# Kernel optimization log

Hardware: AMD Instinct MI355X
Metric: run time of the kernel (lower is better)

Reference implementation:

```python
import jax, jax.numpy as jnp
import numpy as np
from jax import lax

B, K, S = 1, 4, 1024
D = 1024          # hidden_size
DI = 2048         # intermediate_size = 2*D (expand=2)
N = 16            # ssm state size
DT_RANK = 64      # ceil(D/16)
CONV_K = 4
N_LAYERS = 48
CARD = 2048       # vocab
EPS = 1e-5


def setup_inputs() -> dict:
    key = jax.random.key(0)
    ks = jax.random.split(key, 10)
    sc = 0.02
    sequence = jax.random.randint(ks[0], (B, K, S), 0, CARD)
    emb_W = jax.random.normal(ks[1], (K, CARD, D), jnp.float32) * sc
    norm_w = jnp.ones((N_LAYERS, D), jnp.float32)
    in_W = jax.random.normal(ks[2], (N_LAYERS, 2 * DI, D), jnp.float32) * sc
    conv_w = jax.random.normal(ks[3], (N_LAYERS, DI, CONV_K), jnp.float32) * sc
    conv_b = jnp.zeros((N_LAYERS, DI), jnp.float32)
    x_W = jax.random.normal(ks[4], (N_LAYERS, DT_RANK + 2 * N, DI), jnp.float32) * sc
    dt_W = jax.random.normal(ks[5], (N_LAYERS, DI, DT_RANK), jnp.float32) * sc
    dt_b = jax.random.normal(ks[6], (N_LAYERS, DI), jnp.float32) * 0.1
    # HF Mamba init: A_log = log([1..N]) broadcast over channels
    A_log = jnp.log(jnp.broadcast_to(jnp.arange(1, N + 1, dtype=jnp.float32), (N_LAYERS, DI, N)))
    D_skip = jnp.ones((N_LAYERS, DI), jnp.float32)
    out_W = jax.random.normal(ks[7], (N_LAYERS, D, DI), jnp.float32) * sc
    normf_w = jnp.ones((D,), jnp.float32)
    head_W = jax.random.normal(ks[8], (K, CARD, D), jnp.float32) * sc
    head_b = jnp.zeros((K, CARD), jnp.float32)
    return {"sequence": sequence, "emb_W": emb_W, "norm_w": norm_w, "in_W": in_W,
            "conv_w": conv_w, "conv_b": conv_b, "x_W": x_W, "dt_W": dt_W, "dt_b": dt_b,
            "A_log": A_log, "D_skip": D_skip, "out_W": out_W, "normf_w": normf_w,
            "head_W": head_W, "head_b": head_b}


def rmsnorm(x, w):
    return x * lax.rsqrt(jnp.mean(x * x, -1, keepdims=True) + EPS) * w


def mamba_block(x, p):
    """One HF MambaBlock: residual + RMSNorm + MambaMixer (selective scan)."""
    norm_w, in_W, conv_w, conv_b, x_W, dt_W, dt_b, A_log, D_skip, out_W = p
    res = x
    h = rmsnorm(x, norm_w)
    proj = h @ in_W.T                                  # (B,S,2*DI)
    xz, gate = jnp.split(proj, 2, axis=-1)
    # causal depthwise conv1d, kernel 4
    xc = jnp.transpose(xz, (0, 2, 1))                  # (B,DI,S)
    xc = lax.conv_general_dilated(xc, conv_w[:, None, :], (1,), [(CONV_K - 1, 0)],
                                  feature_group_count=DI,
                                  dimension_numbers=("NCH", "OIH", "NCH"))
    xc = xc + conv_b[None, :, None]
    u = jax.nn.silu(jnp.transpose(xc, (0, 2, 1)))      # (B,S,DI)
    ssm_in = u @ x_W.T                                 # (B,S,DT_RANK+2N)
    dt_r, Bm, Cm = jnp.split(ssm_in, [DT_RANK, DT_RANK + N], axis=-1)
    dt = jax.nn.softplus(dt_r @ dt_W.T + dt_b)         # (B,S,DI)
    A = -jnp.exp(A_log)                                # (DI,N)

    def step(hst, inp):
        dt_t, B_t, C_t, u_t = inp                      # (B,DI),(B,N),(B,N),(B,DI)
        dA = jnp.exp(dt_t[:, :, None] * A)             # (B,DI,N)
        hst = dA * hst + (dt_t * u_t)[:, :, None] * B_t[:, None, :]
        y = jnp.einsum("bdn,bn->bd", hst, C_t)
        return hst, y

    h0 = jnp.zeros((B, DI, N), x.dtype)
    _, ys = lax.scan(step, h0, (dt.swapaxes(0, 1), Bm.swapaxes(0, 1),
                                Cm.swapaxes(0, 1), u.swapaxes(0, 1)))
    y = ys.swapaxes(0, 1) + u * D_skip                 # (B,S,DI)
    y = y * jax.nn.silu(gate)
    return res + y @ out_W.T


mamba_block_ckpt = jax.checkpoint(mamba_block)


def reference(sequence, emb_W, norm_w, in_W, conv_w, conv_b, x_W, dt_W, dt_b,
              A_log, D_skip, out_W, normf_w, head_W, head_b):
    # sum of K token-stream embeddings
    x = emb_W[jnp.arange(K)[None, :, None], sequence].sum(1)   # (B,S,D)

    def layer(x, p):
        return mamba_block_ckpt(x, p), None

    x, _ = lax.scan(layer, x, (norm_w, in_W, conv_w, conv_b, x_W, dt_W, dt_b,
                               A_log, D_skip, out_W))
    x = rmsnorm(x, normf_w)
    logits = jnp.einsum("bsd,kvd->bksv", x, head_W) + head_b[None, :, None, :]
    return logits                                              # (B,K,S,CARD)
```

## Files before the change

### kernel.cpp

```cpp
#include <hip/hip_runtime.h>
#include <hip/hip_bf16.h>

#define S 1024
#define D 1024
#define DI 2048
#define NSTATE 16
#define DTR 64
#define XPD 96
#define NL 48
#define CARD 2048
#define KTOK 4

typedef __attribute__((ext_vector_type(8))) short bf16x8;
typedef __attribute__((ext_vector_type(4))) float f32x4;
struct __align__(16) US8 { unsigned long long a, b; };

__device__ __forceinline__ unsigned short f2bf(float f) {
    unsigned u = __builtin_bit_cast(unsigned, f);
    return (unsigned short)((u + 0x7fffu + ((u >> 16) & 1u)) >> 16);
}
__device__ __forceinline__ float bf2f(unsigned short u) {
    return __builtin_bit_cast(float, (unsigned)u << 16);
}
__device__ __forceinline__ float fsilu(float x) { return x / (1.f + __expf(-x)); }
__device__ __forceinline__ float fsoftplus(float x) {
    return fmaxf(x, 0.f) + log1pf(__expf(-fabsf(x)));
}
template<int CTRL>
__device__ __forceinline__ float dpp_add(float v) {
    int m = __builtin_amdgcn_update_dpp(0, __builtin_bit_cast(int, v), CTRL, 0xF, 0xF, true);
    return v + __builtin_bit_cast(float, m);
}
__device__ __forceinline__ void gload_lds16(const void* g, void* l) {
    __builtin_amdgcn_global_load_lds((const __attribute__((address_space(1))) void*)g,
                                     (__attribute__((address_space(3))) void*)l, 16, 0, 0);
}
template<int N> __device__ __forceinline__ void wait_vm() {
    if constexpr (N == 0)      asm volatile("s_waitcnt vmcnt(0)" ::: "memory");
    else if constexpr (N == 3) asm volatile("s_waitcnt vmcnt(3)" ::: "memory");
    else if constexpr (N == 4) asm volatile("s_waitcnt vmcnt(4)" ::: "memory");
    else if constexpr (N == 6) asm volatile("s_waitcnt vmcnt(6)" ::: "memory");
    else                       asm volatile("s_waitcnt vmcnt(8)" ::: "memory");
}

__global__ __launch_bounds__(256) void cvt4_kernel(const float* __restrict__ a, long NA,
                                                   const float* __restrict__ b, long NB,
                                                   const float* __restrict__ c, long NC,
                                                   const float* __restrict__ d, long ND,
                                                   unsigned short* __restrict__ oa,
                                                   unsigned short* __restrict__ ob,
                                                   unsigned short* __restrict__ oc,
                                                   unsigned short* __restrict__ od) {
    long i = (long)blockIdx.x * 256 + threadIdx.x;
    const float* src; unsigned short* dst; long off;
    if (i < NA)                    { src = a; dst = oa; off = i; }
    else if (i < NA + NB)          { src = b; dst = ob; off = i - NA; }
    else if (i < NA + NB + NC)     { src = c; dst = oc; off = i - NA - NB; }
    else                            { src = d; dst = od; off = i - NA - NB - NC; }
    f32x4 v0 = *(const f32x4*)&src[off * 8];
    f32x4 v1 = *(const f32x4*)&src[off * 8 + 4];
    US8 pk;
    pk.a = (unsigned long long)f2bf(v0[0]) | ((unsigned long long)f2bf(v0[1]) << 16)
         | ((unsigned long long)f2bf(v0[2]) << 32) | ((unsigned long long)f2bf(v0[3]) << 48);
    pk.b = (unsigned long long)f2bf(v1[0]) | ((unsigned long long)f2bf(v1[1]) << 16)
         | ((unsigned long long)f2bf(v1[2]) << 32) | ((unsigned long long)f2bf(v1[3]) << 48);
    *(US8*)&dst[off * 8] = pk;
}

__global__ __launch_bounds__(256) void embed_kernel(const int* __restrict__ seq,
                                                    const float* __restrict__ embW,
                                                    float* __restrict__ x) {
    int s = blockIdx.x, t = threadIdx.x;
    f32x4 acc = (f32x4)0.f;
#pragma unroll
    for (int k = 0; k < KTOK; ++k) {
        int tok = seq[k * S + s];
        const f32x4 v = *(const f32x4*)&embW[((size_t)k * CARD + tok) * D + t * 4];
        acc += v;
    }
    *(f32x4*)&x[(size_t)s * D + t * 4] = acc;
}

__global__ __launch_bounds__(256) void rmsnorm_kernel(const float* __restrict__ x,
                                                      const float* __restrict__ w,
                                                      unsigned short* __restrict__ o) {
    int row = blockIdx.x, t = threadIdx.x;
    f32x4 v = *(const f32x4*)&x[(size_t)row * D + t * 4];
    float ss = v[0]*v[0] + v[1]*v[1] + v[2]*v[2] + v[3]*v[3];
#pragma unroll
    for (int off = 32; off >= 1; off >>= 1) ss += __shfl_xor(ss, off);
    __shared__ float red[4];
    int wave = t >> 6, lane = t & 63;
    if (lane == 0) red[wave] = ss;
    __syncthreads();
    ss = red[0] + red[1] + red[2] + red[3];
    float rs = rsqrtf(ss * (1.f / D) + 1e-5f);
    f32x4 wv = *(const f32x4*)&w[t * 4];
    unsigned long long pk = 0;
#pragma unroll
    for (int j = 0; j < 4; ++j)
        pk |= (unsigned long long)f2bf(v[j] * rs * wv[j]) << (16 * j);
    *(unsigned long long*)&o[(size_t)row * D + t * 4] = pk;
}

__global__ __launch_bounds__(256) void outred_rms_kernel(const float* __restrict__ part,
                                                         float* __restrict__ x,
                                                         const float* __restrict__ w,
                                                         unsigned short* __restrict__ o) {
    int row = blockIdx.x, t = threadIdx.x;
    size_t base = (size_t)row * D + t * 4;
    f32x4 v = *(const f32x4*)&x[base];
#pragma unroll
    for (int j = 0; j < 2; ++j)
        v += *(const f32x4*)&part[(size_t)j * (S * D) + base];
    *(f32x4*)&x[base] = v;
    float ss = v[0]*v[0] + v[1]*v[1] + v[2]*v[2] + v[3]*v[3];
#pragma unroll
    for (int off = 32; off >= 1; off >>= 1) ss += __shfl_xor(ss, off);
    __shared__ float red[4];
    int wave = t >> 6, lane = t & 63;
    if (lane == 0) red[wave] = ss;
    __syncthreads();
    ss = red[0] + red[1] + red[2] + red[3];
    float rs = rsqrtf(ss * (1.f / D) + 1e-5f);
    f32x4 wv = *(const f32x4*)&w[t * 4];
    unsigned long long pk = 0;
#pragma unroll
    for (int j = 0; j < 4; ++j)
        pk |= (unsigned long long)f2bf(v[j] * rs * wv[j]) << (16 * j);
    *(unsigned long long*)&o[base] = pk;
}

__global__ __launch_bounds__(256) void ssm_reduce_kernel(const float* __restrict__ part,
                                                         float* __restrict__ ssm,
                                                         unsigned short* __restrict__ ssmb) {
    int i = blockIdx.x * 256 + threadIdx.x;
    float a = 0.f;
#pragma unroll
    for (int j = 0; j < 8; ++j)
        a += part[(size_t)j * (S * XPD) + i];
    ssm[i] = a;
    ssmb[i] = f2bf(a);
}

__global__ __launch_bounds__(256) void conv_silu_kernel(const float* __restrict__ proj,
                                                        const float* __restrict__ cw,
                                                        const float* __restrict__ cb,
                                                        unsigned short* __restrict__ ub) {
    int idx = blockIdx.x * 256 + threadIdx.x;
    int s = idx >> 11, c = idx & (DI - 1);
    f32x4 w = *(const f32x4*)&cw[c * 4];
    float acc = cb[c];
#pragma unroll
    for (int t = 0; t < 4; ++t) {
        int ss = s - 3 + t;
        if (ss >= 0) acc = fmaf(w[t], proj[(size_t)ss * 4096 + c], acc);
    }
    ub[idx] = f2bf(acc * (1.f / (1.f + __expf(-acc))));
}

__global__ __launch_bounds__(1024, 2) void scan2_kernel(const unsigned short* __restrict__ ssmb,
                                                        const unsigned short* __restrict__ dtWb,
                                                        const float* __restrict__ dtb,
                                                        const unsigned short* __restrict__ ub,
                                                        const float* __restrict__ ssm,
                                                        const float* __restrict__ proj,
                                                        const float* __restrict__ A_log,
                                                        const float* __restrict__ Dsk,
                                                        unsigned short* __restrict__ yfb) {
    __shared__ float sdu[S * 4 * 2];
    __shared__ float sP[1024], sQ[1024];

    const int tid = threadIdx.x;
    const int d0 = blockIdx.x * 4;
    const int chunk = tid >> 6;
    const int lane = tid & 63;
    const int dl = (tid >> 4) & 3;
    const int n = tid & 15;
    const int sbase = chunk * 64;

#pragma unroll
    for (int i = 0; i < 4; ++i) {
        int idx = tid + i * 1024;
        int s = idx >> 2, d2 = idx & 3;
        sdu[idx * 2 + 1] = bf2f(ub[(size_t)s * DI + d0 + d2]);
    }

    {
        const int lr = lane & 15;
        const int lk = (lane >> 4) << 3;
        f32x4 dacc[4];
#pragma unroll
        for (int m = 0; m < 4; ++m) dacc[m] = (f32x4)0.f;
        bf16x8 wf0 = *(const bf16x8*)&dtWb[(size_t)(d0 + lr) * DTR + lk];
        bf16x8 wf1 = *(const bf16x8*)&dtWb[(size_t)(d0 + lr) * DTR + 32 + lk];
#pragma unroll
        for (int m = 0; m < 4; ++m) {
            const unsigned short* arow = &ssmb[(size_t)(sbase + m * 16 + lr) * XPD];
            bf16x8 a0 = *(const bf16x8*)&arow[lk];
            bf16x8 a1 = *(const bf16x8*)&arow[32 + lk];
            dacc[m] = __builtin_amdgcn_mfma_f32_16x16x32_bf16(a0, wf0, dacc[m], 0, 0, 0);
            dacc[m] = __builtin_amdgcn_mfma_f32_16x16x32_bf16(a1, wf1, dacc[m], 0, 0, 0);
        }
        if (lr < 4) {
            float bias = dtb[d0 + lr];
            const int rb = (lane >> 4) << 2;
#pragma unroll
            for (int m = 0; m < 4; ++m)
#pragma unroll
                for (int j = 0; j < 4; ++j) {
                    int sl = sbase + m * 16 + rb + j;
                    sdu[(sl * 4 + lr) * 2 + 0] = fsoftplus(dacc[m][j] + bias);
                }
        }
    }
    const float Av = -__expf(A_log[(d0 + dl) * NSTATE + n]);
    const float Dv = Dsk[d0 + dl];
    __syncthreads();

    float h = 0.f, P = 1.f;
#pragma unroll 4
    for (int i = 0; i < 64; ++i) {
        int s = sbase + i;
        float2 du = *(const float2*)&sdu[(s * 4 + dl) * 2];
        float Bs  = ssm[s * XPD + DTR + n];
        float dA  = __expf(du.x * Av);
        P *= dA;
        h = fmaf(dA, h, du.x * du.y * Bs);
    }
    const int pqb = (dl * 16 + n) * 16;
    sP[pqb + chunk] = P;
    sQ[pqb + chunk] = h;
    __syncthreads();
    float hi = 0.f;
    for (int j = 0; j < chunk; ++j) hi = fmaf(sP[pqb + j], hi, sQ[pqb + j]);
    h = hi;
#pragma unroll 2
    for (int i = 0; i < 64; ++i) {
        int s = sbase + i;
        float2 du = *(const float2*)&sdu[(s * 4 + dl) * 2];
        float Bs  = ssm[s * XPD + DTR + n];
        float Cs  = ssm[s * XPD + DTR + NSTATE + n];
        float dA  = __expf(du.x * Av);
        h = fmaf(dA, h, du.x * du.y * Bs);
        float pc = h * Cs;
        pc = dpp_add<0xB1>(pc);
        pc = dpp_add<0x4E>(pc);
        pc = dpp_add<0x124>(pc);
        pc = dpp_add<0x128>(pc);
        if (n == 0) {
            float g = proj[(size_t)s * 4096 + 2048 + d0 + dl];
            yfb[(size_t)s * DI + d0 + dl] = f2bf((pc + du.y * Dv) * fsilu(g));
        }
    }
}

template<int MR, int NR, int EPI, int KSPLIT, int ABF16, int DBUF>
__global__ __launch_bounds__(256) void gemm_bt(const void* __restrict__ Av, int lda,
                                               const unsigned short* __restrict__ W,
                                               float* __restrict__ C,
                                               int K, int N,
                                               const float* __restrict__ bias) {
    constexpr int BM = MR * 32;
    constexpr int BN = NR * 32;
    static_assert(DBUF == 0 || ((BM == 64 || BM == 128) && BN == 128 && ABF16 == 1), "dbuf shape");
    constexpr int NBUF = DBUF ? 3 : 1;
    __shared__ unsigned short As[NBUF][BM][32];
    __shared__ unsigned short Ws[NBUF][BN][32];
    const int tid = threadIdx.x;
    const int lane = tid & 63;
    const int wave = tid >> 6;
    const int wr = wave >> 1, wc = wave & 1;
    const int m0 = blockIdx.y * BM;
    const int n0 = blockIdx.x * BN;
    const unsigned short* Wp = W;
    const float* biasp = bias;
    float* Cp = C;
    if (EPI == 3) {
        size_t z = blockIdx.z;
        Wp += z * (size_t)N * K;
        Cp += z * (size_t)1024 * N;
        biasp += z * N;
    }
    if (EPI == 5)
        Cp = C + (size_t)blockIdx.z * 1024 * N;
    f32x4 acc[MR][NR];
#pragma unroll
    for (int m = 0; m < MR; ++m)
#pragma unroll
        for (int n = 0; n < NR; ++n) acc[m][n] = (f32x4)0.f;

    const int lr = lane & 15;
    const int lk = (lane >> 4) << 3;
    const int grow = lane >> 2;
    const int gcol = (lane & 3) << 3;

    const int kc = (KSPLIT > 1) ? blockIdx.z : 0;
    const int Kc = K / KSPLIT;
    const int kbeg = kc * Kc;

    if constexpr (DBUF) {
        const unsigned short* Ab = (const unsigned short*)Av;
        const int nt = Kc >> 5;
        constexpr int L = BM / 64 + 2;
        auto ISSUE = [&](int t, int buf) {
            const int k0 = kbeg + t * 32;
#pragma unroll
            for (int u2 = wave; u2 < BM / 16; u2 += 4)
                gload_lds16(&Ab[(size_t)(m0 + u2 * 16 + grow) * lda + k0 + gcol],
                            &As[buf][u2 * 16][0]);
#pragma unroll
            for (int u2 = wave; u2 < BN / 16; u2 += 4)
                gload_lds16(&Wp[(size_t)(n0 + u2 * 16 + grow) * K + k0 + gcol],
                            &Ws[buf][u2 * 16][0]);
        };
        ISSUE(0, 0);
        if (nt > 1) ISSUE(1, 1);
        int nb = 2;
        int cb = 0;
        for (int t = 0; t < nt; ++t) {
            if (t + 2 < nt) {
                ISSUE(t + 2, nb);
                if (++nb == 3) nb = 0;
            }
            const int rem = nt - 1 - t;
            if (rem >= 2)      wait_vm<2 * L>();
            else if (rem == 1) wait_vm<L>();
            else               wait_vm<0>();
            __builtin_amdgcn_s_barrier();
            bf16x8 af[MR], wf[NR];
#pragma unroll
            for (int m = 0; m < MR; ++m)
                af[m] = *(const bf16x8*)&As[cb][wr * (MR * 16) + m * 16 + lr][lk];
#pragma unroll
            for (int n = 0; n < NR; ++n)
                wf[n] = *(const bf16x8*)&Ws[cb][wc * (NR * 16) + n * 16 + lr][lk];
            asm volatile("s_waitcnt lgkmcnt(0)" ::: "memory");
            __builtin_amdgcn_s_barrier();
            if (++cb == 3) cb = 0;
#pragma unroll
            for (int m = 0; m < MR; ++m)
#pragma unroll
                for (int n = 0; n < NR; ++n)
                    acc[m][n] = __builtin_amdgcn_mfma_f32_16x16x32_bf16(af[m], wf[n], acc[m][n], 0, 0, 0);
        }
    } else {
        for (int k0 = kbeg; k0 < kbeg + Kc; k0 += 32) {
            __syncthreads();
            if (ABF16) {
                const unsigned short* Ab = (const unsigned short*)Av;
#pragma unroll
                for (int u2 = wave; u2 < BM / 16; u2 += 4)
                    gload_lds16(&Ab[(size_t)(m0 + u2 * 16 + grow) * lda + k0 + gcol],
                                &As[0][u2 * 16][0]);
            } else {
                const float* Af = (const float*)Av;
#pragma unroll
                for (int i = 0; i < BM / 32; ++i) {
                    int idx = tid + i * 256;
                    int row = idx >> 3, c4 = (idx & 7) << 2;
                    f32x4 v = *(const f32x4*)&Af[(size_t)(m0 + row) * lda + k0 + c4];
                    unsigned long long pk = (unsigned long long)f2bf(v[0])
                                          | ((unsigned long long)f2bf(v[1]) << 16)
                                          | ((unsigned long long)f2bf(v[2]) << 32)
                                          | ((unsigned long long)f2bf(v[3]) << 48);
                    *(unsigned long long*)&As[0][row][c4] = pk;
                }
            }
#pragma unroll
            for (int u2 = wave; u2 < BN / 16; u2 += 4)
                gload_lds16(&Wp[(size_t)(n0 + u2 * 16 + grow) * K + k0 + gcol],
                            &Ws[0][u2 * 16][0]);
            __syncthreads();
            bf16x8 af[MR], wf[NR];
#pragma unroll
            for (int m = 0; m < MR; ++m)
                af[m] = *(const bf16x8*)&As[0][wr * (MR * 16) + m * 16 + lr][lk];
#pragma unroll
            for (int n = 0; n < NR; ++n)
                wf[n] = *(const bf16x8*)&Ws[0][wc * (NR * 16) + n * 16 + lr][lk];
#pragma unroll
            for (int m = 0; m < MR; ++m)
#pragma unroll
                for (int n = 0; n < NR; ++n)
                    acc[m][n] = __builtin_amdgcn_mfma_f32_16x16x32_bf16(af[m], wf[n], acc[m][n], 0, 0, 0);
        }
    }

    const int mo = m0 + wr * (MR * 16);
    const int no = n0 + wc * (NR * 16);
    const int rbase = (lane >> 4) << 2;
#pragma unroll
    for (int m = 0; m < MR; ++m) {
#pragma unroll
        for (int n = 0; n < NR; ++n) {
            int col = no + n * 16 + lr;
#pragma unroll
            for (int j = 0; j < 4; ++j) {
                int row = mo + m * 16 + rbase + j;
                float v = acc[m][n][j];
                if (EPI == 1) v = fsoftplus(v + biasp[col]);
                else if (EPI == 3) v += biasp[col];
                Cp[(size_t)row * N + col] = v;
            }
        }
    }
}

#define IN_E   ((size_t)4096 * 1024)
#define OUT_E  ((size_t)1024 * 2048)
#define X_E    ((size_t)XPD * 2048)
#define DT_E   ((size_t)2048 * 64)
#define HEAD_E ((size_t)KTOK * CARD * 1024)

extern "C" void kernel_launch(void* const* d_in, const int* in_sizes, int n_in,
                              void* d_out, int out_size, void* d_ws, size_t ws_size,
                              hipStream_t stream) {
    const int*   seq     = (const int*)d_in[0];
    const float* embW    = (const float*)d_in[1];
    const float* norm_w  = (const float*)d_in[2];
    const float* in_W    = (const float*)d_in[3];
    const float* conv_w  = (const float*)d_in[4];
    const float* conv_b  = (const float*)d_in[5];
    const float* x_W     = (const float*)d_in[6];
    const float* dt_W    = (const float*)d_in[7];
    const float* dt_b    = (const float*)d_in[8];
    const float* A_log   = (const float*)d_in[9];
    const float* D_skip  = (const float*)d_in[10];
    const float* out_W   = (const float*)d_in[11];
    const float* normf_w = (const float*)d_in[12];
    const float* head_W  = (const float*)d_in[13];
    const float* head_b  = (const float*)d_in[14];

    float* ws   = (float*)d_ws;
    float* x    = ws;
    float* proj = x    + (size_t)S * D;
    float* ssm  = proj + (size_t)S * 4096;
    float* xpart = ssm + (size_t)S * 128;
    unsigned short* hnb  = (unsigned short*)(xpart + (size_t)S * DI);
    unsigned short* ub   = hnb  + (size_t)S * D;
    unsigned short* yfb  = ub   + (size_t)S * DI;
    unsigned short* ssmb = yfb  + (size_t)S * DI;
    unsigned short* wbase = ssmb + (size_t)S * 128;
    float* opart = proj;

    size_t actBytes = (char*)wbase - (char*)ws;
    size_t perLayerE = IN_E + OUT_E + X_E + DT_E;
    bool bulk = ws_size >= actBytes + (48 * perLayerE + HEAD_E) * 2 + 256;

    unsigned short* inWb, *outWb, *xWb, *dtWb, *headWb;
    size_t strIn, strOut, strX, strDt;
    if (bulk) {
        inWb  = wbase;
        outWb = inWb  + 48 * IN_E;
        xWb   = outWb + 48 * OUT_E;
        dtWb  = xWb   + 48 * X_E;
        headWb = dtWb + 48 * DT_E;
        strIn = IN_E; strOut = OUT_E; strX = X_E; strDt = DT_E;
    } else {
        inWb  = wbase;
        outWb = inWb  + IN_E;
        xWb   = outWb + OUT_E;
        dtWb  = xWb   + X_E;
        headWb = dtWb + DT_E;
        strIn = strOut = strX = strDt = 0;
    }

    embed_kernel<<<S, 256, 0, stream>>>(seq, embW, x);
    rmsnorm_kernel<<<S, 256, 0, stream>>>(x, norm_w, hnb);
    cvt4_kernel<<<(unsigned)(HEAD_E / 8 / 256), 256, 0, stream>>>(
        head_W, (long)(HEAD_E / 8), nullptr, 0, nullptr, 0, nullptr, 0,
        headWb, nullptr, nullptr, nullptr);
    if (bulk) {
        long na = (long)(48 * IN_E / 8), nb = (long)(48 * OUT_E / 8);
        long nc = (long)(48 * X_E / 8),  nd = (long)(48 * DT_E / 8);
        cvt4_kernel<<<(unsigned)((na + nb + nc + nd) / 256), 256, 0, stream>>>(
            in_W, na, out_W, nb, x_W, nc, dt_W, nd, inWb, outWb, xWb, dtWb);
    }

    for (int l = 0; l < NL; ++l) {
        if (!bulk) {
            cvt4_kernel<<<(unsigned)(perLayerE / 8 / 256), 256, 0, stream>>>(
                in_W + (size_t)l * IN_E, (long)(IN_E / 8),
                out_W + (size_t)l * OUT_E, (long)(OUT_E / 8),
                x_W + (size_t)l * X_E, (long)(X_E / 8),
                dt_W + (size_t)l * DT_E, (long)(DT_E / 8),
                inWb, outWb, xWb, dtWb);
        }
        gemm_bt<2, 4, 0, 1, 1, 1><<<dim3(32, 16), 256, 0, stream>>>(hnb, D,
            inWb + (size_t)l * strIn, proj, D, 4096, nullptr);
        conv_silu_kernel<<<(S * DI) / 256, 256, 0, stream>>>(proj,
            conv_w + (size_t)l * DI * 4, conv_b + (size_t)l * DI, ub);
        gemm_bt<2, 3, 5, 8, 1, 0><<<dim3(1, 16, 8), 256, 0, stream>>>(ub, DI,
            xWb + (size_t)l * strX, xpart, DI, XPD, nullptr);
        ssm_reduce_kernel<<<(S * XPD) / 256, 256, 0, stream>>>(xpart, ssm, ssmb);
        scan2_kernel<<<DI / 4, 1024, 0, stream>>>(ssmb, dtWb + (size_t)l * strDt,
            dt_b + (size_t)l * DI, ub, ssm, proj,
            A_log + (size_t)l * DI * NSTATE, D_skip + (size_t)l * DI, yfb);
        gemm_bt<2, 4, 5, 2, 1, 1><<<dim3(8, 16, 2), 256, 0, stream>>>(yfb, DI,
            outWb + (size_t)l * strOut, opart, DI, D, nullptr);
        outred_rms_kernel<<<S, 256, 0, stream>>>(opart, x,
            (l + 1 < NL) ? (norm_w + (size_t)(l + 1) * D) : normf_w, hnb);
    }

    gemm_bt<4, 4, 3, 1, 1, 1><<<dim3(16, 8, 4), 256, 0, stream>>>(hnb, D, headWb,
        (float*)d_out, D, CARD, head_b);
}
```

Before: 7.394 ms.

## Swizzle GEMM LDS layout, vectorize scan I/O, raise x-proj split-K

XOR-swizzles the GEMM shared-memory tile layout for both the async weight loads and the fp32 A-staging path, aiming to remove LDS bank conflicts on the fragment reads. The scan kernel now loads its u slice with one vector load per thread, and buffers y in shared memory so the gated output is written as packed 4-wide stores instead of scattered single-lane stores. The x-projection split-K goes from 8 to 16 chunks for more parallelism, at the cost of a larger partial buffer to reduce. The outred kernel gains separate input and output pointers, but it is still called in place.

```diff
diff --git a/kernel.cpp b/kernel.cpp
--- a/kernel.cpp
+++ b/kernel.cpp
@@ -13,6 +13,7 @@
 
 typedef __attribute__((ext_vector_type(8))) short bf16x8;
 typedef __attribute__((ext_vector_type(4))) float f32x4;
+typedef __attribute__((ext_vector_type(4))) unsigned short us4;
 struct __align__(16) US8 { unsigned long long a, b; };
 
 __device__ __forceinline__ unsigned short f2bf(float f) {
@@ -104,16 +105,17 @@
 }
 
 __global__ __launch_bounds__(256) void outred_rms_kernel(const float* __restrict__ part,
-                                                         float* __restrict__ x,
+                                                         const float* __restrict__ xin,
+                                                         float* __restrict__ xout,
                                                          const float* __restrict__ w,
                                                          unsigned short* __restrict__ o) {
     int row = blockIdx.x, t = threadIdx.x;
     size_t base = (size_t)row * D + t * 4;
-    f32x4 v = *(const f32x4*)&x[base];
+    f32x4 v = *(const f32x4*)&xin[base];
 #pragma unroll
     for (int j = 0; j < 2; ++j)
         v += *(const f32x4*)&part[(size_t)j * (S * D) + base];
-    *(f32x4*)&x[base] = v;
+    *(f32x4*)&xout[base] = v;
     float ss = v[0]*v[0] + v[1]*v[1] + v[2]*v[2] + v[3]*v[3];
 #pragma unroll
     for (int off = 32; off >= 1; off >>= 1) ss += __shfl_xor(ss, off);
@@ -137,7 +139,7 @@
     int i = blockIdx.x * 256 + threadIdx.x;
     float a = 0.f;
 #pragma unroll
-    for (int j = 0; j < 8; ++j)
+    for (int j = 0; j < 16; ++j)
         a += part[(size_t)j * (S * XPD) + i];
     ssm[i] = a;
     ssmb[i] = f2bf(a);
@@ -170,6 +172,7 @@
                                                         unsigned short* __restrict__ yfb) {
     __shared__ float sdu[S * 4 * 2];
     __shared__ float sP[1024], sQ[1024];
+    __shared__ float sy[S * 4];
 
     const int tid = threadIdx.x;
     const int d0 = blockIdx.x * 4;
@@ -179,11 +182,11 @@
     const int n = tid & 15;
     const int sbase = chunk * 64;
 
-#pragma unroll
-    for (int i = 0; i < 4; ++i) {
-        int idx = tid + i * 1024;
-        int s = idx >> 2, d2 = idx & 3;
-        sdu[idx * 2 + 1] = bf2f(ub[(size_t)s * DI + d0 + d2]);
+    {
+        us4 uv = *(const us4*)&ub[(size_t)tid * DI + d0];
+#pragma unroll
+        for (int j = 0; j < 4; ++j)
+            sdu[(tid * 4 + j) * 2 + 1] = bf2f(uv[j]);
     }
 
     {
@@ -248,10 +251,19 @@
         pc = dpp_add<0x4E>(pc);
         pc = dpp_add<0x124>(pc);
         pc = dpp_add<0x128>(pc);
-        if (n == 0) {
-            float g = proj[(size_t)s * 4096 + 2048 + d0 + dl];
-            yfb[(size_t)s * DI + d0 + dl] = f2bf((pc + du.y * Dv) * fsilu(g));
-        }
+        if (n == 0)
+            sy[s * 4 + dl] = pc + du.y * Dv;
+    }
+    __syncthreads();
+    {
+        int s = tid;
+        f32x4 yv = *(const f32x4*)&sy[s * 4];
+        f32x4 g  = *(const f32x4*)&proj[(size_t)s * 4096 + 2048 + d0];
+        unsigned long long pk = 0;
+#pragma unroll
+        for (int j = 0; j < 4; ++j)
+            pk |= (unsigned long long)f2bf(yv[j] * fsilu(g[j])) << (16 * j);
+        *(unsigned long long*)&yfb[(size_t)s * DI + d0] = pk;
     }
 }
 
@@ -291,9 +303,9 @@
         for (int n = 0; n < NR; ++n) acc[m][n] = (f32x4)0.f;
 
     const int lr = lane & 15;
-    const int lk = (lane >> 4) << 3;
+    const int lkp = (((lane >> 4) ^ ((lr >> 1) & 3)) << 3);
     const int grow = lane >> 2;
-    const int gcol = (lane & 3) << 3;
+    const int gcol = (((lane & 3) ^ ((lane >> 3) & 3)) << 3);
 
     const int kc = (KSPLIT > 1) ? blockIdx.z : 0;
     const int Kc = K / KSPLIT;
@@ -317,7 +329,7 @@
         ISSUE(0, 0);
         if (nt > 1) ISSUE(1, 1);
         int nb = 2;
-        int cb = 0;
+        int cb2 = 0;
         for (int t = 0; t < nt; ++t) {
             if (t + 2 < nt) {
                 ISSUE(t + 2, nb);
@@ -331,13 +343,13 @@
             bf16x8 af[MR], wf[NR];
 #pragma unroll
             for (int m = 0; m < MR; ++m)
-                af[m] = *(const bf16x8*)&As[cb][wr * (MR * 16) + m * 16 + lr][lk];
+                af[m] = *(const bf16x8*)&As[cb2][wr * (MR * 16) + m * 16 + lr][lkp];
 #pragma unroll
             for (int n = 0; n < NR; ++n)
-                wf[n] = *(const bf16x8*)&Ws[cb][wc * (NR * 16) + n * 16 + lr][lk];
+                wf[n] = *(const bf16x8*)&Ws[cb2][wc * (NR * 16) + n * 16 + lr][lkp];
             asm volatile("s_waitcnt lgkmcnt(0)" ::: "memory");
             __builtin_amdgcn_s_barrier();
-            if (++cb == 3) cb = 0;
+            if (++cb2 == 3) cb2 = 0;
 #pragma unroll
             for (int m = 0; m < MR; ++m)
 #pragma unroll
@@ -364,7 +376,9 @@
                                           | ((unsigned long long)f2bf(v[1]) << 16)
                                           | ((unsigned long long)f2bf(v[2]) << 32)
                                           | ((unsigned long long)f2bf(v[3]) << 48);
-                    *(unsigned long long*)&As[0][row][c4] = pk;
+                    int sl = (idx & 7) >> 1, hf = (idx & 7) & 1;
+                    int p = sl ^ ((row >> 1) & 3);
+                    *(unsigned long long*)&As[0][row][p * 8 + hf * 4] = pk;
                 }
             }
 #pragma unroll
@@ -375,10 +389,10 @@
             bf16x8 af[MR], wf[NR];
 #pragma unroll
             for (int m = 0; m < MR; ++m)
-                af[m] = *(const bf16x8*)&As[0][wr * (MR * 16) + m * 16 + lr][lk];
+                af[m] = *(const bf16x8*)&As[0][wr * (MR * 16) + m * 16 + lr][lkp];
 #pragma unroll
             for (int n = 0; n < NR; ++n)
-                wf[n] = *(const bf16x8*)&Ws[0][wc * (NR * 16) + n * 16 + lr][lk];
+                wf[n] = *(const bf16x8*)&Ws[0][wc * (NR * 16) + n * 16 + lr][lkp];
 #pragma unroll
             for (int m = 0; m < MR; ++m)
 #pragma unroll
@@ -491,7 +505,7 @@
             inWb + (size_t)l * strIn, proj, D, 4096, nullptr);
         conv_silu_kernel<<<(S * DI) / 256, 256, 0, stream>>>(proj,
             conv_w + (size_t)l * DI * 4, conv_b + (size_t)l * DI, ub);
-        gemm_bt<2, 3, 5, 8, 1, 0><<<dim3(1, 16, 8), 256, 0, stream>>>(ub, DI,
+        gemm_bt<2, 3, 5, 16, 1, 0><<<dim3(1, 16, 16), 256, 0, stream>>>(ub, DI,
             xWb + (size_t)l * strX, xpart, DI, XPD, nullptr);
         ssm_reduce_kernel<<<(S * XPD) / 256, 256, 0, stream>>>(xpart, ssm, ssmb);
         scan2_kernel<<<DI / 4, 1024, 0, stream>>>(ssmb, dtWb + (size_t)l * strDt,
@@ -499,7 +513,7 @@
             A_log + (size_t)l * DI * NSTATE, D_skip + (size_t)l * DI, yfb);
         gemm_bt<2, 4, 5, 2, 1, 1><<<dim3(8, 16, 2), 256, 0, stream>>>(yfb, DI,
             outWb + (size_t)l * strOut, opart, DI, D, nullptr);
-        outred_rms_kernel<<<S, 256, 0, stream>>>(opart, x,
+        outred_rms_kernel<<<S, 256, 0, stream>>>(opart, x, x,
             (l + 1 < NL) ? (norm_w + (size_t)(l + 1) * D) : normf_w, hnb);
     }
 
```

Measured after the change: 6.543 ms. -11.5%, faster.
